# Performance work log

Hardware: AMD Instinct MI355X
Metric: run time of the kernel (lower is better)

Reference implementation:

```python
import jax, jax.numpy as jnp
import numpy as np

NUM_SINK = 8   # cfg.SINKHORN_ITERS
MASS = 0.9     # marginal value used for a and b


def _graph_conv(x, W_enc, b_enc, W1, b1, W2, b2, k):
    # Node encoder
    h = jax.nn.relu(x @ W_enc + b_enc)                       # [G,M,D]
    # kNN in embedding space (per graph)
    sq = jnp.sum(h * h, axis=-1)                             # [G,M]
    d2 = sq[:, :, None] + sq[:, None, :] - 2.0 * jnp.einsum('gmd,gnd->gmn', h, h)
    d2 = d2 + jnp.eye(h.shape[1], dtype=h.dtype) * 1e9       # exclude self-loop
    _, idx = jax.lax.top_k(-d2, k)                           # [G,M,k]
    neigh = jax.vmap(lambda hg, ig: hg[ig])(h, idx)          # [G,M,k,D]
    hc = jnp.broadcast_to(h[:, :, None, :], neigh.shape)
    e = jnp.concatenate([hc, neigh - hc], axis=-1)           # [G,M,k,2D]
    e = jax.nn.relu(e @ W1 + b1)                             # edge embed
    e = e @ W2 + b2                                          # back to D
    return jnp.max(e, axis=2)                                # max-aggregate over neighbors


def _sinkhorn(cost, lam):
    # log-domain unrolled Sinkhorn, batched over graphs; a=b=0.9 marginals
    log_p = -cost / lam                                      # [G,M,N]
    log_m = jnp.log(jnp.asarray(MASS, cost.dtype))
    for _ in range(NUM_SINK - 1):
        log_p = log_p - (jax.nn.logsumexp(log_p, axis=2, keepdims=True) - log_m)
        log_p = log_p - (jax.nn.logsumexp(log_p, axis=1, keepdims=True) - log_m)
    log_p = log_p - (jax.nn.logsumexp(log_p, axis=2, keepdims=True) - log_m)
    return jnp.exp(log_p)


def setup_inputs() -> dict:
    key = jax.random.key(0)
    ks = jax.random.split(key, 6)
    G, M, D = 64, 256, 256
    E = 256  # edge embed size
    inp = {
        'tra_x': jax.random.normal(ks[0], (G, M, D), jnp.float32),
        'det_x': jax.random.normal(ks[1], (G, M, D), jnp.float32),
        'W_enc': jax.random.normal(ks[2], (D, D), jnp.float32) / np.sqrt(D),
        'b_enc': jnp.zeros((D,), jnp.float32),
        'W1': jax.random.normal(ks[3], (2 * D, E), jnp.float32) / np.sqrt(2 * D),
        'b1': jnp.zeros((E,), jnp.float32),
        'W2': jax.random.normal(ks[4], (E, D), jnp.float32) / np.sqrt(E),
        'b2': jnp.zeros((D,), jnp.float32),
        'eplison': jnp.zeros((1,), jnp.float32),
        'k': 16,
    }
    return inp


def reference(tra_x, det_x, W_enc, b_enc, W1, b1, W2, b2, eplison, k):
    tra = _graph_conv(tra_x, W_enc, b_enc, W1, b1, W2, b2, k)  # [G,M,D]
    det = _graph_conv(det_x, W_enc, b_enc, W1, b1, W2, b2, k)  # [G,N,D]
    corr = jnp.einsum('gmd,gnd->gmn', tra, det)
    n1 = jnp.linalg.norm(tra, axis=-1)                         # [G,M]
    n2 = jnp.linalg.norm(det, axis=-1)                         # [G,N]
    cost = -corr / (n1[:, :, None] * n2[:, None, :])
    lam = jnp.exp(eplison[0]) + 0.03
    return _sinkhorn(cost, lam)                                # [G,M,N]
```

## Files before the change

### kernel.cpp

```cpp
#include <hip/hip_runtime.h>
#include <math.h>

#define NG 64
#define NM 256
#define ND 256
#define NK 16
#define NR (NG * NM)
#define NB 16

#define MASSF 0.9f

typedef __attribute__((ext_vector_type(8))) short bf16x8;
typedef __attribute__((ext_vector_type(4))) float f32x4;

static __device__ __forceinline__ short f2bf(float x) {
  union {
    float f;
    unsigned u;
  } v;
  v.f = x;
  unsigned r = v.u + 0x7FFFu + ((v.u >> 16) & 1u);
  return (short)(r >> 16);
}
static __device__ __forceinline__ float bf2f(short x) {
  union {
    unsigned u;
    float f;
  } v;
  v.u = ((unsigned)(unsigned short)x) << 16;
  return v.f;
}

__global__ __launch_bounds__(256) void prep_k(const float* __restrict__ W1,
                                              const float* __restrict__ b1,
                                              const float* __restrict__ W2,
                                              short* __restrict__ w2t, short* __restrict__ w1cat,
                                              float* __restrict__ biascat) {
  const int b = blockIdx.x, k = threadIdx.x;
  if (b < 256) {
    w2t[b * 256 + k] = f2bf(W2[(size_t)k * 256 + b]);
  } else {
    const int n = b - 256;
    float v;
    if (n < 256)
      v = W1[(size_t)k * 256 + n] - W1[(size_t)(k + 256) * 256 + n];
    else
      v = W1[(size_t)(k + 256) * 256 + (n - 256)];
    w1cat[(size_t)n * 256 + k] = f2bf(v);
    if (k == 0) biascat[n] = (n < 256) ? b1[n] : 0.f;
  }
}

__global__ __launch_bounds__(256) void gemm_nn2_k(const float* __restrict__ A,
                                                  const float* __restrict__ B,
                                                  const float* __restrict__ bias,
                                                  float* __restrict__ C,
                                                  short* __restrict__ Cbf) {
  __shared__ float As[2][16][68];
  __shared__ float Bs[2][16][128];
  const int tid = threadIdx.x;
  const int tx = tid & 15, ty = tid >> 4;
  const int m0 = blockIdx.y * 64, n0 = blockIdx.x * 128;
  const int arow = tid >> 2, akc = (tid & 3) * 4;
  const int bkr = tid >> 4, bcc = (tid & 15) * 4;
  float4 av, bv0, bv1;
  float acc[4][8] = {};
  auto gload = [&](int k0) {
    av = *(const float4*)&A[(size_t)(m0 + arow) * 256 + k0 + akc];
    bv0 = *(const float4*)&B[(size_t)(k0 + bkr) * 256 + n0 + bcc];
    bv1 = *(const float4*)&B[(size_t)(k0 + bkr) * 256 + n0 + 64 + bcc];
  };
  auto swrite = [&](int buf) {
    As[buf][akc + 0][arow] = av.x;
    As[buf][akc + 1][arow] = av.y;
    As[buf][akc + 2][arow] = av.z;
    As[buf][akc + 3][arow] = av.w;
    *(float4*)&Bs[buf][bkr][bcc] = bv0;
    *(float4*)&Bs[buf][bkr][64 + bcc] = bv1;
  };
  gload(0);
  swrite(0);
  __syncthreads();
  for (int s = 0; s < 16; ++s) {
    if (s < 15) gload((s + 1) * 16);
    const int buf = s & 1;
#pragma unroll
    for (int kk = 0; kk < 16; ++kk) {
      const float4 a0 = *(const float4*)&As[buf][kk][ty * 4];
      const float4 b0 = *(const float4*)&Bs[buf][kk][tx * 4];
      const float4 b1 = *(const float4*)&Bs[buf][kk][64 + tx * 4];
      const float aa[4] = {a0.x, a0.y, a0.z, a0.w};
      const float bb[8] = {b0.x, b0.y, b0.z, b0.w, b1.x, b1.y, b1.z, b1.w};
#pragma unroll
      for (int i = 0; i < 4; ++i)
#pragma unroll
        for (int j = 0; j < 8; ++j) acc[i][j] = fmaf(aa[i], bb[j], acc[i][j]);
    }
    if (s < 15) swrite((s + 1) & 1);
    __syncthreads();
  }
  const float4 bia0 = *(const float4*)&bias[n0 + tx * 4];
  const float4 bia1 = *(const float4*)&bias[n0 + 64 + tx * 4];
#pragma unroll
  for (int i = 0; i < 4; ++i) {
    const size_t row = (size_t)(m0 + ty * 4 + i);
    float4 o0 = {fmaxf(acc[i][0] + bia0.x, 0.f), fmaxf(acc[i][1] + bia0.y, 0.f),
                 fmaxf(acc[i][2] + bia0.z, 0.f), fmaxf(acc[i][3] + bia0.w, 0.f)};
    float4 o1 = {fmaxf(acc[i][4] + bia1.x, 0.f), fmaxf(acc[i][5] + bia1.y, 0.f),
                 fmaxf(acc[i][6] + bia1.z, 0.f), fmaxf(acc[i][7] + bia1.w, 0.f)};
    *(float4*)&C[row * 256 + n0 + tx * 4] = o0;
    *(float4*)&C[row * 256 + n0 + 64 + tx * 4] = o1;
    short4 h0 = {f2bf(o0.x), f2bf(o0.y), f2bf(o0.z), f2bf(o0.w)};
    short4 h1 = {f2bf(o1.x), f2bf(o1.y), f2bf(o1.z), f2bf(o1.w)};
    *(short4*)&Cbf[row * 256 + n0 + tx * 4] = h0;
    *(short4*)&Cbf[row * 256 + n0 + 64 + tx * 4] = h1;
  }
}

__global__ __launch_bounds__(256) void gemm_nt2_k(const float* __restrict__ h,
                                                  float* __restrict__ C) {
  const int flat0 = blockIdx.x + 2 * (blockIdx.y + 4 * blockIdx.z);
  const int flat = ((flat0 & 7) << 6) | (flat0 >> 3);
  const int bx = flat & 1, by = (flat >> 1) & 3, g = flat >> 3;
  if (bx == 0 && by >= 2) return;
  __shared__ float As[2][16][68];
  __shared__ float Bs[2][16][128];
  const float* Ag = h + (size_t)g * NM * ND;
  float* Cg = C + (size_t)g * NM * NM;
  const int tid = threadIdx.x;
  const int tx = tid & 15, ty = tid >> 4;
  const int m0 = by * 64, n0 = bx * 128;
  const int arow = tid >> 2, akc = (tid & 3) * 4;
  const int brow = tid >> 1, bkc = (tid & 1) * 8;
  float4 av, bva, bvb;
  float acc[4][8] = {};
  auto gload = [&](int k0) {
    av = *(const float4*)&Ag[(size_t)(m0 + arow) * 256 + k0 + akc];
    bva = *(const float4*)&Ag[(size_t)(n0 + brow) * 256 + k0 + bkc];
    bvb = *(const float4*)&Ag[(size_t)(n0 + brow) * 256 + k0 + bkc + 4];
  };
  auto swrite = [&](int buf) {
    As[buf][akc + 0][arow] = av.x;
    As[buf][akc + 1][arow] = av.y;
    As[buf][akc + 2][arow] = av.z;
    As[buf][akc + 3][arow] = av.w;
    Bs[buf][bkc + 0][brow] = bva.x;
    Bs[buf][bkc + 1][brow] = bva.y;
    Bs[buf][bkc + 2][brow] = bva.z;
    Bs[buf][bkc + 3][brow] = bva.w;
    Bs[buf][bkc + 4][brow] = bvb.x;
    Bs[buf][bkc + 5][brow] = bvb.y;
    Bs[buf][bkc + 6][brow] = bvb.z;
    Bs[buf][bkc + 7][brow] = bvb.w;
  };
  gload(0);
  swrite(0);
  __syncthreads();
  for (int s = 0; s < 16; ++s) {
    if (s < 15) gload((s + 1) * 16);
    const int buf = s & 1;
#pragma unroll
    for (int kk = 0; kk < 16; ++kk) {
      const float4 a0 = *(const float4*)&As[buf][kk][ty * 4];
      const float4 b0 = *(const float4*)&Bs[buf][kk][tx * 4];
      const float4 b1 = *(const float4*)&Bs[buf][kk][64 + tx * 4];
      const float aa[4] = {a0.x, a0.y, a0.z, a0.w};
      const float bb[8] = {b0.x, b0.y, b0.z, b0.w, b1.x, b1.y, b1.z, b1.w};
#pragma unroll
      for (int i = 0; i < 4; ++i)
#pragma unroll
        for (int j = 0; j < 8; ++j) acc[i][j] = fmaf(aa[i], bb[j], acc[i][j]);
    }
    if (s < 15) swrite((s + 1) & 1);
    __syncthreads();
  }
#pragma unroll
  for (int i = 0; i < 4; ++i) {
    const size_t row = (size_t)(m0 + ty * 4 + i);
    float4 o0 = {acc[i][0], acc[i][1], acc[i][2], acc[i][3]};
    float4 o1 = {acc[i][4], acc[i][5], acc[i][6], acc[i][7]};
    *(float4*)&Cg[row * 256 + n0 + tx * 4] = o0;
    *(float4*)&Cg[row * 256 + n0 + 64 + tx * 4] = o1;
  }
  if (bx == 1 && by < 2) {
#pragma unroll
    for (int j = 0; j < 4; ++j) {
      const size_t col0 = (size_t)(n0 + tx * 4 + j);
      const size_t col1 = (size_t)(n0 + 64 + tx * 4 + j);
      float4 t0 = {acc[0][j], acc[1][j], acc[2][j], acc[3][j]};
      float4 t1 = {acc[0][4 + j], acc[1][4 + j], acc[2][4 + j], acc[3][4 + j]};
      *(float4*)&Cg[col0 * 256 + m0 + ty * 4] = t0;
      *(float4*)&Cg[col1 * 256 + m0 + ty * 4] = t1;
    }
  }
}

__global__ __launch_bounds__(256) void diag_k(const float* __restrict__ S,
                                              float* __restrict__ sq) {
  const int g = blockIdx.x, m = threadIdx.x;
  sq[g * 256 + m] = S[(size_t)g * NM * NM + (size_t)m * 257];
}

__global__ __launch_bounds__(256, 2) void mlp1_mfma_k(const short* __restrict__ A,
                                                      const short* __restrict__ Bt,
                                                      const float* __restrict__ biascat,
                                                      short* __restrict__ baseb,
                                                      short* __restrict__ n1b) {
  __shared__ char As[64 * 512];
  const int tid = threadIdx.x;
  const int l = tid & 63, wv = tid >> 6;
  const int r = l & 15, gq = l >> 4;
  const int m0 = blockIdx.y * 64, n0 = blockIdx.x * 128;
  bf16x8 bfr[2][8];
  float bv[2];
#pragma unroll
  for (int nt = 0; nt < 2; ++nt) {
    const int col = n0 + wv * 32 + nt * 16 + r;
    const short* wb = Bt + (size_t)col * 256 + gq * 8;
#pragma unroll
    for (int ks = 0; ks < 8; ++ks) bfr[nt][ks] = *(const bf16x8*)(wb + ks * 32);
    bv[nt] = biascat[col];
  }
  const int row = tid >> 2, ch = tid & 3;
  const char* ag = (const char*)(A + (size_t)(m0 + row) * 256) + ch * 128;
  char* lb = As + row * 512;
#pragma unroll
  for (int j = 0; j < 8; ++j)
    *(bf16x8*)(lb + (((ch * 128 + j * 16)) ^ ((row & 7) << 4))) = *(const bf16x8*)(ag + j * 16);
  __syncthreads();
  f32x4 acc[4][2];
#pragma unroll
  for (int mt = 0; mt < 4; ++mt)
#pragma unroll
    for (int nt = 0; nt < 2; ++nt) acc[mt][nt] = (f32x4){0.f, 0.f, 0.f, 0.f};
#pragma unroll
  for (int ks = 0; ks < 8; ++ks) {
    bf16x8 a[4];
#pragma unroll
    for (int mt = 0; mt < 4; ++mt)
      a[mt] = *(const bf16x8*)(As + (mt * 16 + r) * 512 + ((gq * 16 + ks * 64) ^ ((r & 7) << 4)));
#pragma unroll
    for (int mt = 0; mt < 4; ++mt)
#pragma unroll
      for (int nt = 0; nt < 2; ++nt)
        acc[mt][nt] = __builtin_amdgcn_mfma_f32_16x16x32_bf16(a[mt], bfr[nt][ks], acc[mt][nt], 0, 0, 0);
  }
  short* dst = (n0 < 256) ? baseb : n1b;
  const int cb = (n0 < 256) ? n0 : n0 - 256;
#pragma unroll
  for (int mt = 0; mt < 4; ++mt)
#pragma unroll
    for (int nt = 0; nt < 2; ++nt) {
      const int col = cb + wv * 32 + nt * 16 + r;
#pragma unroll
      for (int reg = 0; reg < 4; ++reg) {
        const int rw = m0 + mt * 16 + gq * 4 + reg;
        dst[(size_t)rw * 256 + col] = f2bf(acc[mt][nt][reg] + bv[nt]);
      }
    }
}

__global__ __launch_bounds__(256, 2) void cost_mfma_k(const short* __restrict__ featT,
                                                      const short* __restrict__ featD,
                                                      const float* __restrict__ nA,
                                                      const float* __restrict__ nB,
                                                      const float* __restrict__ eps,
                                                      float* __restrict__ P) {
  __shared__ char As[64 * 512];
  const int g = blockIdx.z;
  const short* A = featT + (size_t)g * NM * ND;
  const short* Bt = featD + (size_t)g * NM * ND;
  const int tid = threadIdx.x;
  const int l = tid & 63, wv = tid >> 6;
  const int r = l & 15, gq = l >> 4;
  const int m0 = blockIdx.y * 64, n0 = blockIdx.x * 128;
  bf16x8 bfr[2][8];
  float rnb[2];
#pragma unroll
  for (int nt = 0; nt < 2; ++nt) {
    const int col = n0 + wv * 32 + nt * 16 + r;
    const short* wb = Bt + (size_t)col * 256 + gq * 8;
#pragma unroll
    for (int ks = 0; ks < 8; ++ks) bfr[nt][ks] = *(const bf16x8*)(wb + ks * 32);
    rnb[nt] = 1.0f / nB[g * NM + col];
  }
  const int row = tid >> 2, ch = tid & 3;
  const char* ag = (const char*)(A + (size_t)(m0 + row) * 256) + ch * 128;
  char* lb = As + row * 512;
#pragma unroll
  for (int j = 0; j < 8; ++j)
    *(bf16x8*)(lb + (((ch * 128 + j * 16)) ^ ((row & 7) << 4))) = *(const bf16x8*)(ag + j * 16);
  __syncthreads();
  f32x4 acc[4][2];
#pragma unroll
  for (int mt = 0; mt < 4; ++mt)
#pragma unroll
    for (int nt = 0; nt < 2; ++nt) acc[mt][nt] = (f32x4){0.f, 0.f, 0.f, 0.f};
#pragma unroll
  for (int ks = 0; ks < 8; ++ks) {
    bf16x8 a[4];
#pragma unroll
    for (int mt = 0; mt < 4; ++mt)
      a[mt] = *(const bf16x8*)(As + (mt * 16 + r) * 512 + ((gq * 16 + ks * 64) ^ ((r & 7) << 4)));
#pragma unroll
    for (int mt = 0; mt < 4; ++mt)
#pragma unroll
      for (int nt = 0; nt < 2; ++nt)
        acc[mt][nt] = __builtin_amdgcn_mfma_f32_16x16x32_bf16(a[mt], bfr[nt][ks], acc[mt][nt], 0, 0, 0);
  }
  const float inv_lam = 1.0f / (expf(eps[0]) + 0.03f);
#pragma unroll
  for (int mt = 0; mt < 4; ++mt) {
    float ria[4];
#pragma unroll
    for (int reg = 0; reg < 4; ++reg)
      ria[reg] = inv_lam / nA[g * NM + m0 + mt * 16 + gq * 4 + reg];
#pragma unroll
    for (int nt = 0; nt < 2; ++nt) {
      const int col = n0 + wv * 32 + nt * 16 + r;
#pragma unroll
      for (int reg = 0; reg < 4; ++reg) {
        const int rw = m0 + mt * 16 + gq * 4 + reg;
        P[(size_t)g * NM * NM + (size_t)rw * 256 + col] =
            expf(acc[mt][nt][reg] * ria[reg] * rnb[nt]);
      }
    }
  }
}

__global__ __launch_bounds__(256) void normrow_bf_k(const short* __restrict__ feat,
                                                    float* __restrict__ nrm) {
  const int w = threadIdx.x >> 6, lane = threadIdx.x & 63;
  const int row = blockIdx.x * 4 + w;
  const short4 v = *(const short4*)&feat[(size_t)row * ND + lane * 4];
  const float a = bf2f(v.x), b = bf2f(v.y), c = bf2f(v.z), d = bf2f(v.w);
  float s = a * a + b * b + c * c + d * d;
#pragma unroll
  for (int off = 32; off; off >>= 1) s += __shfl_xor(s, off);
  if (lane == 0) nrm[row] = sqrtf(s);
}

__global__ __launch_bounds__(256) void topk_k(const float* __restrict__ S,
                                              const float* __restrict__ sq,
                                              int* __restrict__ idx) {
  const int w = threadIdx.x >> 6, lane = threadIdx.x & 63;
  const int row = blockIdx.x * 4 + w;
  const int g = row >> 8, m = row & 255;
  const float* Srow = S + (size_t)row * NM;
  const float* sqg = sq + g * NM;
  const float sm = sqg[m];
  const float4 sv = *(const float4*)&Srow[lane * 4];
  const float4 qv = *(const float4*)&sqg[lane * 4];
  float cand[4] = {sm + qv.x - 2.f * sv.x, sm + qv.y - 2.f * sv.y, sm + qv.z - 2.f * sv.z,
                   sm + qv.w - 2.f * sv.w};
#pragma unroll
  for (int t = 0; t < 4; ++t)
    if (lane * 4 + t == m) cand[t] = 1e30f;
  for (int rnd = 0; rnd < NK; ++rnd) {
    float bvv = cand[0];
    int bi = lane * 4;
#pragma unroll
    for (int t = 1; t < 4; ++t)
      if (cand[t] < bvv) {
        bvv = cand[t];
        bi = lane * 4 + t;
      }
#pragma unroll
    for (int off = 1; off < 64; off <<= 1) {
      const float ov = __shfl_xor(bvv, off);
      const int oi = __shfl_xor(bi, off);
      if (ov < bvv || (ov == bvv && oi < bi)) {
        bvv = ov;
        bi = oi;
      }
    }
    if (lane == 0) idx[(size_t)row * NK + rnd] = bi;
    if ((bi >> 2) == lane) cand[bi & 3] = 1e30f;
  }
}

__global__ __launch_bounds__(512, 4) void edgemlp_mfma7_k(
    const short* __restrict__ baseb, const short* __restrict__ n1b, const int* __restrict__ idx,
    const short* __restrict__ w2t, const float* __restrict__ b2, short* __restrict__ featbf) {
  __shared__ short E[2][2][512 * 8];
  __shared__ int sidx[NB * NK];
  const int tid = threadIdx.x;
  const int l = tid & 63, wv = tid >> 6;
  const int blk = ((blockIdx.x & 7) << 7) | (blockIdx.x >> 3);
  const int node0 = blk * NB;
  const int g = node0 >> 8;
  const int r = l & 15, gq = l >> 4;
  if (tid < NB * NK) sidx[tid] = idx[(size_t)node0 * NK + tid];
  bf16x8 bfr[2][8];
  float b2v[2];
#pragma unroll
  for (int t = 0; t < 2; ++t) {
    const int nb = wv * 2 + t;
    const short* wb = w2t + (size_t)(nb * 16 + r) * 256 + gq * 8;
#pragma unroll
    for (int ks = 0; ks < 8; ++ks) bfr[t][ks] = *(const bf16x8*)(wb + ks * 32);
    b2v[t] = b2[nb * 16 + r];
  }
  __syncthreads();
  const int r_s = tid & 15;
  const int col_s = ((tid >> 6) * 32) + (((tid >> 4) & 3) * 8);
  bf16x8 bs0, ns0, bs1, ns1;
  auto sload = [&](int s) {
    const int na = s * 2;
    bs0 = *(const bf16x8*)(baseb + (((size_t)(node0 + na)) << 8) + col_s);
    ns0 = *(const bf16x8*)(n1b + ((((size_t)g << 8) + sidx[na * NK + r_s]) << 8) + col_s);
    bs1 = *(const bf16x8*)(baseb + (((size_t)(node0 + na + 1)) << 8) + col_s);
    ns1 = *(const bf16x8*)(n1b + ((((size_t)g << 8) + sidx[(na + 1) * NK + r_s]) << 8) + col_s);
  };
  auto swrite = [&](int s) {
    const int buf = s & 1;
    bf16x8 w0, w1;
#pragma unroll
    for (int q = 0; q < 8; ++q) {
      w0[q] = f2bf(fmaxf(bf2f(bs0[q]) + bf2f(ns0[q]), 0.f));
      w1[q] = f2bf(fmaxf(bf2f(bs1[q]) + bf2f(ns1[q]), 0.f));
    }
    *(bf16x8*)&E[buf][0][tid * 8] = w0;
    *(bf16x8*)&E[buf][1][tid * 8] = w1;
  };
  sload(0);
  swrite(0);
  __syncthreads();
  for (int s = 0; s < NB / 2; ++s) {
    if (s + 1 < NB / 2) sload(s + 1);
    const int buf = s & 1;
#pragma unroll
    for (int q = 0; q < 2; ++q) {
      const short* eb = &E[buf][q][0];
      f32x4 acc0 = (f32x4){0.f, 0.f, 0.f, 0.f};
      f32x4 acc1 = (f32x4){0.f, 0.f, 0.f, 0.f};
#pragma unroll
      for (int ks = 0; ks < 8; ++ks) {
        const bf16x8 a = *(const bf16x8*)(eb + ks * 512 + l * 8);
        acc0 = __builtin_amdgcn_mfma_f32_16x16x32_bf16(a, bfr[0][ks], acc0, 0, 0, 0);
        acc1 = __builtin_amdgcn_mfma_f32_16x16x32_bf16(a, bfr[1][ks], acc1, 0, 0, 0);
      }
      const int nd = node0 + s * 2 + q;
      float m0v = fmaxf(fmaxf(acc0[0], acc0[1]), fmaxf(acc0[2], acc0[3]));
      m0v = fmaxf(m0v, __shfl_xor(m0v, 16));
      m0v = fmaxf(m0v, __shfl_xor(m0v, 32));
      float m1v = fmaxf(fmaxf(acc1[0], acc1[1]), fmaxf(acc1[2], acc1[3]));
      m1v = fmaxf(m1v, __shfl_xor(m1v, 16));
      m1v = fmaxf(m1v, __shfl_xor(m1v, 32));
      if (gq == 0) {
        featbf[((size_t)nd << 8) + (wv * 2 + 0) * 16 + r] = f2bf(m0v + b2v[0]);
        featbf[((size_t)nd << 8) + (wv * 2 + 1) * 16 + r] = f2bf(m1v + b2v[1]);
      }
    }
    if (s + 1 < NB / 2) swrite(s + 1);
    __syncthreads();
  }
}

__global__ __launch_bounds__(1024) void sinkhorn_k(float* __restrict__ P) {
  __shared__ float red[16][256];
  __shared__ float scal[256];
  const int t = threadIdx.x;
  const int tc = t & 15;
  const int trw = t >> 4;
  const int wv = t >> 6, l = t & 63;
  float* Pg = P + (size_t)blockIdx.x * NM * NM;
  float p[4][16];
#pragma unroll
  for (int i = 0; i < 4; ++i)
#pragma unroll
    for (int q = 0; q < 4; ++q)
      *(f32x4*)&p[i][q * 4] = *(const f32x4*)&Pg[(size_t)(trw * 4 + i) * NM + tc * 16 + q * 4];

  auto rowpass = [&]() {
#pragma unroll
    for (int i = 0; i < 4; ++i) {
      float s = p[i][0];
#pragma unroll
      for (int j = 1; j < 16; ++j) s += p[i][j];
      s += __shfl_xor(s, 1);
      s += __shfl_xor(s, 2);
      s += __shfl_xor(s, 4);
      s += __shfl_xor(s, 8);
      const float sc = MASSF / s;
#pragma unroll
      for (int j = 0; j < 16; ++j) p[i][j] *= sc;
    }
  };
  auto colpass = [&]() {
    float tmp[16];
#pragma unroll
    for (int j = 0; j < 16; ++j) tmp[j] = ((p[0][j] + p[1][j]) + (p[2][j] + p[3][j]));
#pragma unroll
    for (int j = 0; j < 16; ++j) {
      tmp[j] += __shfl_xor(tmp[j], 16);
      tmp[j] += __shfl_xor(tmp[j], 32);
    }
    if (l < 16) {
#pragma unroll
      for (int q = 0; q < 4; ++q)
        *(f32x4*)&red[wv][l * 16 + q * 4] = *(const f32x4*)&tmp[q * 4];
    }
    __syncthreads();
    if (t < 256) {
      float s = red[0][t];
#pragma unroll
      for (int w = 1; w < 16; ++w) s += red[w][t];
      scal[t] = MASSF / s;
    }
    __syncthreads();
#pragma unroll
    for (int j = 0; j < 16; ++j) {
      const float sc = scal[tc * 16 + j];
#pragma unroll
      for (int i = 0; i < 4; ++i) p[i][j] *= sc;
    }
    __syncthreads();
  };
  for (int it = 0; it < 7; ++it) {
    rowpass();
    colpass();
  }
  rowpass();
#pragma unroll
  for (int i = 0; i < 4; ++i)
#pragma unroll
    for (int q = 0; q < 4; ++q)
      *(f32x4*)&Pg[(size_t)(trw * 4 + i) * NM + tc * 16 + q * 4] = *(const f32x4*)&p[i][q * 4];
}

extern "C" void kernel_launch(void* const* d_in, const int* in_sizes, int n_in, void* d_out,
                              int out_size, void* d_ws, size_t ws_size, hipStream_t stream) {
  const float* tra_x = (const float*)d_in[0];
  const float* det_x = (const float*)d_in[1];
  const float* W_enc = (const float*)d_in[2];
  const float* b_enc = (const float*)d_in[3];
  const float* W1 = (const float*)d_in[4];
  const float* b1 = (const float*)d_in[5];
  const float* W2 = (const float*)d_in[6];
  const float* b2 = (const float*)d_in[7];
  const float* eps = (const float*)d_in[8];
  float* out = (float*)d_out;

  const size_t SZ = (size_t)NR * ND;
  float* h = (float*)d_ws;
  short* hbf = (short*)(h + SZ);
  short* baseb = hbf + SZ;
  short* n1b = baseb + SZ;
  short* featT = n1b + SZ;
  short* featD = featT + SZ;
  float* sq = (float*)(featD + SZ);
  float* nT = sq + NR;
  float* nD = nT + NR;
  int* idx = (int*)(nD + NR);
  short* w2t = (short*)(idx + (size_t)NR * NK);
  short* w1cat = w2t + 256 * 256;
  float* biascat = (float*)(w1cat + 512 * 256);
  float* S = out;

  const float* xs[2] = {tra_x, det_x};
  short* feats[2] = {featT, featD};
  float* nrms[2] = {nT, nD};

  prep_k<<<768, 256, 0, stream>>>(W1, b1, W2, w2t, w1cat, biascat);
  for (int s2 = 0; s2 < 2; ++s2) {
    gemm_nn2_k<<<dim3(2, 256), 256, 0, stream>>>(xs[s2], W_enc, b_enc, h, hbf);
    mlp1_mfma_k<<<dim3(4, 256), 256, 0, stream>>>(hbf, w1cat, biascat, baseb, n1b);
    gemm_nt2_k<<<dim3(2, 4, NG), 256, 0, stream>>>(h, S);
    diag_k<<<NG, 256, 0, stream>>>(S, sq);
    topk_k<<<4096, 256, 0, stream>>>(S, sq, idx);
    edgemlp_mfma7_k<<<NR / NB, 512, 0, stream>>>(baseb, n1b, idx, w2t, b2, feats[s2]);
    normrow_bf_k<<<4096, 256, 0, stream>>>(feats[s2], nrms[s2]);
  }
  cost_mfma_k<<<dim3(2, 4, NG), 256, 0, stream>>>(featT, featD, nT, nD, eps, out);
  sinkhorn_k<<<NG, 1024, 0, stream>>>(out);
}
```

Baseline: 404.6 us.

## Switch MFMA path to fp16, fuse diag and row-norm kernels, widen edge blocks

Converts every bf16 intermediate and MFMA op to fp16. The edge ReLU now uses packed v_pk_add/v_pk_max f16 instructions instead of per-element bf16 unpack and repack. The diagonal extraction moves into the NT gemm epilogue, and the feature row norms are computed inside the edge-MLP kernel, removing the diag_k and normrow kernels (four launches and their memory passes). The edge-MLP block also processes 32 nodes instead of 16, which halves the grid and amortizes the per-block weight loads. fp16 has a narrower range than bf16, which could affect accuracy if intermediate values grow large.

```diff
diff --git a/kernel.cpp b/kernel.cpp
--- a/kernel.cpp
+++ b/kernel.cpp
@@ -6,39 +6,31 @@
 #define ND 256
 #define NK 16
 #define NR (NG * NM)
-#define NB 16
+#define NB 32
 
 #define MASSF 0.9f
 
-typedef __attribute__((ext_vector_type(8))) short bf16x8;
+typedef _Float16 f16;
+typedef __attribute__((ext_vector_type(8))) _Float16 f16x8;
+typedef __attribute__((ext_vector_type(4))) _Float16 f16x4;
 typedef __attribute__((ext_vector_type(4))) float f32x4;
-
-static __device__ __forceinline__ short f2bf(float x) {
-  union {
-    float f;
-    unsigned u;
-  } v;
-  v.f = x;
-  unsigned r = v.u + 0x7FFFu + ((v.u >> 16) & 1u);
-  return (short)(r >> 16);
-}
-static __device__ __forceinline__ float bf2f(short x) {
-  union {
-    unsigned u;
-    float f;
-  } v;
-  v.u = ((unsigned)(unsigned short)x) << 16;
-  return v.f;
+typedef __attribute__((ext_vector_type(4))) unsigned u32x4;
+
+static __device__ __forceinline__ unsigned pkrelu(unsigned a, unsigned b) {
+  unsigned r;
+  asm("v_pk_add_f16 %0, %1, %2" : "=v"(r) : "v"(a), "v"(b));
+  asm("v_pk_max_f16 %0, %1, %2" : "=v"(r) : "v"(r), "v"(0u));
+  return r;
 }
 
 __global__ __launch_bounds__(256) void prep_k(const float* __restrict__ W1,
                                               const float* __restrict__ b1,
                                               const float* __restrict__ W2,
-                                              short* __restrict__ w2t, short* __restrict__ w1cat,
+                                              f16* __restrict__ w2t, f16* __restrict__ w1cat,
                                               float* __restrict__ biascat) {
   const int b = blockIdx.x, k = threadIdx.x;
   if (b < 256) {
-    w2t[b * 256 + k] = f2bf(W2[(size_t)k * 256 + b]);
+    w2t[b * 256 + k] = (f16)W2[(size_t)k * 256 + b];
   } else {
     const int n = b - 256;
     float v;
@@ -46,7 +38,7 @@
       v = W1[(size_t)k * 256 + n] - W1[(size_t)(k + 256) * 256 + n];
     else
       v = W1[(size_t)(k + 256) * 256 + (n - 256)];
-    w1cat[(size_t)n * 256 + k] = f2bf(v);
+    w1cat[(size_t)n * 256 + k] = (f16)v;
     if (k == 0) biascat[n] = (n < 256) ? b1[n] : 0.f;
   }
 }
@@ -55,7 +47,7 @@
                                                   const float* __restrict__ B,
                                                   const float* __restrict__ bias,
                                                   float* __restrict__ C,
-                                                  short* __restrict__ Cbf) {
+                                                  f16* __restrict__ Cf) {
   __shared__ float As[2][16][68];
   __shared__ float Bs[2][16][128];
   const int tid = threadIdx.x;
@@ -110,15 +102,16 @@
                  fmaxf(acc[i][6] + bia1.z, 0.f), fmaxf(acc[i][7] + bia1.w, 0.f)};
     *(float4*)&C[row * 256 + n0 + tx * 4] = o0;
     *(float4*)&C[row * 256 + n0 + 64 + tx * 4] = o1;
-    short4 h0 = {f2bf(o0.x), f2bf(o0.y), f2bf(o0.z), f2bf(o0.w)};
-    short4 h1 = {f2bf(o1.x), f2bf(o1.y), f2bf(o1.z), f2bf(o1.w)};
-    *(short4*)&Cbf[row * 256 + n0 + tx * 4] = h0;
-    *(short4*)&Cbf[row * 256 + n0 + 64 + tx * 4] = h1;
+    f16x4 h0 = {(f16)o0.x, (f16)o0.y, (f16)o0.z, (f16)o0.w};
+    f16x4 h1 = {(f16)o1.x, (f16)o1.y, (f16)o1.z, (f16)o1.w};
+    *(f16x4*)&Cf[row * 256 + n0 + tx * 4] = h0;
+    *(f16x4*)&Cf[row * 256 + n0 + 64 + tx * 4] = h1;
   }
 }
 
 __global__ __launch_bounds__(256) void gemm_nt2_k(const float* __restrict__ h,
-                                                  float* __restrict__ C) {
+                                                  float* __restrict__ C,
+                                                  float* __restrict__ sq) {
   const int flat0 = blockIdx.x + 2 * (blockIdx.y + 4 * blockIdx.z);
   const int flat = ((flat0 & 7) << 6) | (flat0 >> 3);
   const int bx = flat & 1, by = (flat >> 1) & 3, g = flat >> 3;
@@ -174,13 +167,16 @@
     if (s < 15) swrite((s + 1) & 1);
     __syncthreads();
   }
+  const int c0 = n0 + tx * 4, c1 = n0 + 64 + tx * 4;
 #pragma unroll
   for (int i = 0; i < 4; ++i) {
-    const size_t row = (size_t)(m0 + ty * 4 + i);
+    const int row = m0 + ty * 4 + i;
     float4 o0 = {acc[i][0], acc[i][1], acc[i][2], acc[i][3]};
     float4 o1 = {acc[i][4], acc[i][5], acc[i][6], acc[i][7]};
-    *(float4*)&Cg[row * 256 + n0 + tx * 4] = o0;
-    *(float4*)&Cg[row * 256 + n0 + 64 + tx * 4] = o1;
+    *(float4*)&Cg[(size_t)row * 256 + c0] = o0;
+    *(float4*)&Cg[(size_t)row * 256 + c1] = o1;
+    if (row >= c0 && row < c0 + 4) sq[g * 256 + row] = acc[i][row - c0];
+    if (row >= c1 && row < c1 + 4) sq[g * 256 + row] = acc[i][4 + row - c1];
   }
   if (bx == 1 && by < 2) {
 #pragma unroll
@@ -195,30 +191,24 @@
   }
 }
 
-__global__ __launch_bounds__(256) void diag_k(const float* __restrict__ S,
-                                              float* __restrict__ sq) {
-  const int g = blockIdx.x, m = threadIdx.x;
-  sq[g * 256 + m] = S[(size_t)g * NM * NM + (size_t)m * 257];
-}
-
-__global__ __launch_bounds__(256, 2) void mlp1_mfma_k(const short* __restrict__ A,
-                                                      const short* __restrict__ Bt,
+__global__ __launch_bounds__(256, 2) void mlp1_mfma_k(const f16* __restrict__ A,
+                                                      const f16* __restrict__ Bt,
                                                       const float* __restrict__ biascat,
-                                                      short* __restrict__ baseb,
-                                                      short* __restrict__ n1b) {
+                                                      f16* __restrict__ baseb,
+                                                      f16* __restrict__ n1b) {
   __shared__ char As[64 * 512];
   const int tid = threadIdx.x;
   const int l = tid & 63, wv = tid >> 6;
   const int r = l & 15, gq = l >> 4;
   const int m0 = blockIdx.y * 64, n0 = blockIdx.x * 128;
-  bf16x8 bfr[2][8];
+  f16x8 bfr[2][8];
   float bv[2];
 #pragma unroll
   for (int nt = 0; nt < 2; ++nt) {
     const int col = n0 + wv * 32 + nt * 16 + r;
-    const short* wb = Bt + (size_t)col * 256 + gq * 8;
-#pragma unroll
-    for (int ks = 0; ks < 8; ++ks) bfr[nt][ks] = *(const bf16x8*)(wb + ks * 32);
+    const f16* wb = Bt + (size_t)col * 256 + gq * 8;
+#pragma unroll
+    for (int ks = 0; ks < 8; ++ks) bfr[nt][ks] = *(const f16x8*)(wb + ks * 32);
     bv[nt] = biascat[col];
   }
   const int row = tid >> 2, ch = tid & 3;
@@ -226,7 +216,7 @@
   char* lb = As + row * 512;
 #pragma unroll
   for (int j = 0; j < 8; ++j)
-    *(bf16x8*)(lb + (((ch * 128 + j * 16)) ^ ((row & 7) << 4))) = *(const bf16x8*)(ag + j * 16);
+    *(f16x8*)(lb + (((ch * 128 + j * 16)) ^ ((row & 7) << 4))) = *(const f16x8*)(ag + j * 16);
   __syncthreads();
   f32x4 acc[4][2];
 #pragma unroll
@@ -235,17 +225,17 @@
     for (int nt = 0; nt < 2; ++nt) acc[mt][nt] = (f32x4){0.f, 0.f, 0.f, 0.f};
 #pragma unroll
   for (int ks = 0; ks < 8; ++ks) {
-    bf16x8 a[4];
+    f16x8 a[4];
 #pragma unroll
     for (int mt = 0; mt < 4; ++mt)
-      a[mt] = *(const bf16x8*)(As + (mt * 16 + r) * 512 + ((gq * 16 + ks * 64) ^ ((r & 7) << 4)));
+      a[mt] = *(const f16x8*)(As + (mt * 16 + r) * 512 + ((gq * 16 + ks * 64) ^ ((r & 7) << 4)));
 #pragma unroll
     for (int mt = 0; mt < 4; ++mt)
 #pragma unroll
       for (int nt = 0; nt < 2; ++nt)
-        acc[mt][nt] = __builtin_amdgcn_mfma_f32_16x16x32_bf16(a[mt], bfr[nt][ks], acc[mt][nt], 0, 0, 0);
-  }
-  short* dst = (n0 < 256) ? baseb : n1b;
+        acc[mt][nt] = __builtin_amdgcn_mfma_f32_16x16x32_f16(a[mt], bfr[nt][ks], acc[mt][nt], 0, 0, 0);
+  }
+  f16* dst = (n0 < 256) ? baseb : n1b;
   const int cb = (n0 < 256) ? n0 : n0 - 256;
 #pragma unroll
   for (int mt = 0; mt < 4; ++mt)
@@ -255,33 +245,33 @@
 #pragma unroll
       for (int reg = 0; reg < 4; ++reg) {
         const int rw = m0 + mt * 16 + gq * 4 + reg;
-        dst[(size_t)rw * 256 + col] = f2bf(acc[mt][nt][reg] + bv[nt]);
+        dst[(size_t)rw * 256 + col] = (f16)(acc[mt][nt][reg] + bv[nt]);
       }
     }
 }
 
-__global__ __launch_bounds__(256, 2) void cost_mfma_k(const short* __restrict__ featT,
-                                                      const short* __restrict__ featD,
+__global__ __launch_bounds__(256, 2) void cost_mfma_k(const f16* __restrict__ featT,
+                                                      const f16* __restrict__ featD,
                                                       const float* __restrict__ nA,
                                                       const float* __restrict__ nB,
                                                       const float* __restrict__ eps,
                                                       float* __restrict__ P) {
   __shared__ char As[64 * 512];
   const int g = blockIdx.z;
-  const short* A = featT + (size_t)g * NM * ND;
-  const short* Bt = featD + (size_t)g * NM * ND;
+  const f16* A = featT + (size_t)g * NM * ND;
+  const f16* Bt = featD + (size_t)g * NM * ND;
   const int tid = threadIdx.x;
   const int l = tid & 63, wv = tid >> 6;
   const int r = l & 15, gq = l >> 4;
   const int m0 = blockIdx.y * 64, n0 = blockIdx.x * 128;
-  bf16x8 bfr[2][8];
+  f16x8 bfr[2][8];
   float rnb[2];
 #pragma unroll
   for (int nt = 0; nt < 2; ++nt) {
     const int col = n0 + wv * 32 + nt * 16 + r;
-    const short* wb = Bt + (size_t)col * 256 + gq * 8;
-#pragma unroll
-    for (int ks = 0; ks < 8; ++ks) bfr[nt][ks] = *(const bf16x8*)(wb + ks * 32);
+    const f16* wb = Bt + (size_t)col * 256 + gq * 8;
+#pragma unroll
+    for (int ks = 0; ks < 8; ++ks) bfr[nt][ks] = *(const f16x8*)(wb + ks * 32);
     rnb[nt] = 1.0f / nB[g * NM + col];
   }
   const int row = tid >> 2, ch = tid & 3;
@@ -289,7 +279,7 @@
   char* lb = As + row * 512;
 #pragma unroll
   for (int j = 0; j < 8; ++j)
-    *(bf16x8*)(lb + (((ch * 128 + j * 16)) ^ ((row & 7) << 4))) = *(const bf16x8*)(ag + j * 16);
+    *(f16x8*)(lb + (((ch * 128 + j * 16)) ^ ((row & 7) << 4))) = *(const f16x8*)(ag + j * 16);
   __syncthreads();
   f32x4 acc[4][2];
 #pragma unroll
@@ -298,15 +288,15 @@
     for (int nt = 0; nt < 2; ++nt) acc[mt][nt] = (f32x4){0.f, 0.f, 0.f, 0.f};
 #pragma unroll
   for (int ks = 0; ks < 8; ++ks) {
-    bf16x8 a[4];
+    f16x8 a[4];
 #pragma unroll
     for (int mt = 0; mt < 4; ++mt)
-      a[mt] = *(const bf16x8*)(As + (mt * 16 + r) * 512 + ((gq * 16 + ks * 64) ^ ((r & 7) << 4)));
+      a[mt] = *(const f16x8*)(As + (mt * 16 + r) * 512 + ((gq * 16 + ks * 64) ^ ((r & 7) << 4)));
 #pragma unroll
     for (int mt = 0; mt < 4; ++mt)
 #pragma unroll
       for (int nt = 0; nt < 2; ++nt)
-        acc[mt][nt] = __builtin_amdgcn_mfma_f32_16x16x32_bf16(a[mt], bfr[nt][ks], acc[mt][nt], 0, 0, 0);
+        acc[mt][nt] = __builtin_amdgcn_mfma_f32_16x16x32_f16(a[mt], bfr[nt][ks], acc[mt][nt], 0, 0, 0);
   }
   const float inv_lam = 1.0f / (expf(eps[0]) + 0.03f);
 #pragma unroll
@@ -326,18 +316,6 @@
       }
     }
   }
-}
-
-__global__ __launch_bounds__(256) void normrow_bf_k(const short* __restrict__ feat,
-                                                    float* __restrict__ nrm) {
-  const int w = threadIdx.x >> 6, lane = threadIdx.x & 63;
-  const int row = blockIdx.x * 4 + w;
-  const short4 v = *(const short4*)&feat[(size_t)row * ND + lane * 4];
-  const float a = bf2f(v.x), b = bf2f(v.y), c = bf2f(v.z), d = bf2f(v.w);
-  float s = a * a + b * b + c * c + d * d;
-#pragma unroll
-  for (int off = 32; off; off >>= 1) s += __shfl_xor(s, off);
-  if (lane == 0) nrm[row] = sqrtf(s);
 }
 
 __global__ __launch_bounds__(256) void topk_k(const float* __restrict__ S,
@@ -379,49 +357,51 @@
   }
 }
 
-__global__ __launch_bounds__(512, 4) void edgemlp_mfma7_k(
-    const short* __restrict__ baseb, const short* __restrict__ n1b, const int* __restrict__ idx,
-    const short* __restrict__ w2t, const float* __restrict__ b2, short* __restrict__ featbf) {
-  __shared__ short E[2][2][512 * 8];
+__global__ __launch_bounds__(512, 4) void edgemlp_mfma8_k(
+    const f16* __restrict__ baseb, const f16* __restrict__ n1b, const int* __restrict__ idx,
+    const f16* __restrict__ w2t, const float* __restrict__ b2, f16* __restrict__ featf,
+    float* __restrict__ nrm) {
+  __shared__ unsigned E[2][2][512 * 4];
   __shared__ int sidx[NB * NK];
+  __shared__ float normp[NB][8];
   const int tid = threadIdx.x;
   const int l = tid & 63, wv = tid >> 6;
-  const int blk = ((blockIdx.x & 7) << 7) | (blockIdx.x >> 3);
+  const int blk = ((blockIdx.x & 7) << 6) | (blockIdx.x >> 3);
   const int node0 = blk * NB;
   const int g = node0 >> 8;
   const int r = l & 15, gq = l >> 4;
-  if (tid < NB * NK) sidx[tid] = idx[(size_t)node0 * NK + tid];
-  bf16x8 bfr[2][8];
+  sidx[tid] = idx[(size_t)node0 * NK + tid];
+  f16x8 bfr[2][8];
   float b2v[2];
 #pragma unroll
   for (int t = 0; t < 2; ++t) {
     const int nb = wv * 2 + t;
-    const short* wb = w2t + (size_t)(nb * 16 + r) * 256 + gq * 8;
-#pragma unroll
-    for (int ks = 0; ks < 8; ++ks) bfr[t][ks] = *(const bf16x8*)(wb + ks * 32);
+    const f16* wb = w2t + (size_t)(nb * 16 + r) * 256 + gq * 8;
+#pragma unroll
+    for (int ks = 0; ks < 8; ++ks) bfr[t][ks] = *(const f16x8*)(wb + ks * 32);
     b2v[t] = b2[nb * 16 + r];
   }
   __syncthreads();
   const int r_s = tid & 15;
   const int col_s = ((tid >> 6) * 32) + (((tid >> 4) & 3) * 8);
-  bf16x8 bs0, ns0, bs1, ns1;
+  u32x4 bs0, ns0, bs1, ns1;
   auto sload = [&](int s) {
     const int na = s * 2;
-    bs0 = *(const bf16x8*)(baseb + (((size_t)(node0 + na)) << 8) + col_s);
-    ns0 = *(const bf16x8*)(n1b + ((((size_t)g << 8) + sidx[na * NK + r_s]) << 8) + col_s);
-    bs1 = *(const bf16x8*)(baseb + (((size_t)(node0 + na + 1)) << 8) + col_s);
-    ns1 = *(const bf16x8*)(n1b + ((((size_t)g << 8) + sidx[(na + 1) * NK + r_s]) << 8) + col_s);
+    bs0 = *(const u32x4*)(baseb + (((size_t)(node0 + na)) << 8) + col_s);
+    ns0 = *(const u32x4*)(n1b + ((((size_t)g << 8) + sidx[na * NK + r_s]) << 8) + col_s);
+    bs1 = *(const u32x4*)(baseb + (((size_t)(node0 + na + 1)) << 8) + col_s);
+    ns1 = *(const u32x4*)(n1b + ((((size_t)g << 8) + sidx[(na + 1) * NK + r_s]) << 8) + col_s);
   };
   auto swrite = [&](int s) {
     const int buf = s & 1;
-    bf16x8 w0, w1;
-#pragma unroll
-    for (int q = 0; q < 8; ++q) {
-      w0[q] = f2bf(fmaxf(bf2f(bs0[q]) + bf2f(ns0[q]), 0.f));
-      w1[q] = f2bf(fmaxf(bf2f(bs1[q]) + bf2f(ns1[q]), 0.f));
-    }
-    *(bf16x8*)&E[buf][0][tid * 8] = w0;
-    *(bf16x8*)&E[buf][1][tid * 8] = w1;
+    u32x4 w0, w1;
+#pragma unroll
+    for (int q = 0; q < 4; ++q) {
+      w0[q] = pkrelu(bs0[q], ns0[q]);
+      w1[q] = pkrelu(bs1[q], ns1[q]);
+    }
+    *(u32x4*)&E[buf][0][tid * 4] = w0;
+    *(u32x4*)&E[buf][1][tid * 4] = w1;
   };
   sload(0);
   swrite(0);
@@ -431,14 +411,14 @@
     const int buf = s & 1;
 #pragma unroll
     for (int q = 0; q < 2; ++q) {
-      const short* eb = &E[buf][q][0];
+      const char* eb = (const char*)&E[buf][q][0];
       f32x4 acc0 = (f32x4){0.f, 0.f, 0.f, 0.f};
       f32x4 acc1 = (f32x4){0.f, 0.f, 0.f, 0.f};
 #pragma unroll
       for (int ks = 0; ks < 8; ++ks) {
-        const bf16x8 a = *(const bf16x8*)(eb + ks * 512 + l * 8);
-        acc0 = __builtin_amdgcn_mfma_f32_16x16x32_bf16(a, bfr[0][ks], acc0, 0, 0, 0);
-        acc1 = __builtin_amdgcn_mfma_f32_16x16x32_bf16(a, bfr[1][ks], acc1, 0, 0, 0);
+        const f16x8 a = *(const f16x8*)(eb + ks * 1024 + l * 16);
+        acc0 = __builtin_amdgcn_mfma_f32_16x16x32_f16(a, bfr[0][ks], acc0, 0, 0, 0);
+        acc1 = __builtin_amdgcn_mfma_f32_16x16x32_f16(a, bfr[1][ks], acc1, 0, 0, 0);
       }
       const int nd = node0 + s * 2 + q;
       float m0v = fmaxf(fmaxf(acc0[0], acc0[1]), fmaxf(acc0[2], acc0[3]));
@@ -447,13 +427,28 @@
       float m1v = fmaxf(fmaxf(acc1[0], acc1[1]), fmaxf(acc1[2], acc1[3]));
       m1v = fmaxf(m1v, __shfl_xor(m1v, 16));
       m1v = fmaxf(m1v, __shfl_xor(m1v, 32));
+      const f16 h0 = (f16)(m0v + b2v[0]);
+      const f16 h1 = (f16)(m1v + b2v[1]);
       if (gq == 0) {
-        featbf[((size_t)nd << 8) + (wv * 2 + 0) * 16 + r] = f2bf(m0v + b2v[0]);
-        featbf[((size_t)nd << 8) + (wv * 2 + 1) * 16 + r] = f2bf(m1v + b2v[1]);
+        featf[((size_t)nd << 8) + (wv * 2 + 0) * 16 + r] = h0;
+        featf[((size_t)nd << 8) + (wv * 2 + 1) * 16 + r] = h1;
       }
+      const float o0 = (float)h0, o1 = (float)h1;
+      float ss = o0 * o0 + o1 * o1;
+      ss += __shfl_xor(ss, 1);
+      ss += __shfl_xor(ss, 2);
+      ss += __shfl_xor(ss, 4);
+      ss += __shfl_xor(ss, 8);
+      if (l == 0) normp[s * 2 + q][wv] = ss;
     }
     if (s + 1 < NB / 2) swrite(s + 1);
     __syncthreads();
+  }
+  if (tid < NB) {
+    float s = 0.f;
+#pragma unroll
+    for (int w = 0; w < 8; ++w) s += normp[tid][w];
+    nrm[node0 + tid] = sqrtf(s);
   }
 }
 
@@ -544,33 +539,31 @@
 
   const size_t SZ = (size_t)NR * ND;
   float* h = (float*)d_ws;
-  short* hbf = (short*)(h + SZ);
-  short* baseb = hbf + SZ;
-  short* n1b = baseb + SZ;
-  short* featT = n1b + SZ;
-  short* featD = featT + SZ;
+  f16* hf = (f16*)(h + SZ);
+  f16* baseb = hf + SZ;
+  f16* n1b = baseb + SZ;
+  f16* featT = n1b + SZ;
+  f16* featD = featT + SZ;
   float* sq = (float*)(featD + SZ);
   float* nT = sq + NR;
   float* nD = nT + NR;
   int* idx = (int*)(nD + NR);
-  short* w2t = (short*)(idx + (size_t)NR * NK);
-  short* w1cat = w2t + 256 * 256;
+  f16* w2t = (f16*)(idx + (size_t)NR * NK);
+  f16* w1cat = w2t + 256 * 256;
   float* biascat = (float*)(w1cat + 512 * 256);
   float* S = out;
 
   const float* xs[2] = {tra_x, det_x};
-  short* feats[2] = {featT, featD};
+  f16* feats[2] = {featT, featD};
   float* nrms[2] = {nT, nD};
 
   prep_k<<<768, 256, 0, stream>>>(W1, b1, W2, w2t, w1cat, biascat);
   for (int s2 = 0; s2 < 2; ++s2) {
-    gemm_nn2_k<<<dim3(2, 256), 256, 0, stream>>>(xs[s2], W_enc, b_enc, h, hbf);
-    mlp1_mfma_k<<<dim3(4, 256), 256, 0, stream>>>(hbf, w1cat, biascat, baseb, n1b);
-    gemm_nt2_k<<<dim3(2, 4, NG), 256, 0, stream>>>(h, S);
-    diag_k<<<NG, 256, 0, stream>>>(S, sq);
+    gemm_nn2_k<<<dim3(2, 256), 256, 0, stream>>>(xs[s2], W_enc, b_enc, h, hf);
+    mlp1_mfma_k<<<dim3(4, 256), 256, 0, stream>>>(hf, w1cat, biascat, baseb, n1b);
+    gemm_nt2_k<<<dim3(2, 4, NG), 256, 0, stream>>>(h, S, sq);
     topk_k<<<4096, 256, 0, stream>>>(S, sq, idx);
-    edgemlp_mfma7_k<<<NR / NB, 512, 0, stream>>>(baseb, n1b, idx, w2t, b2, feats[s2]);
-    normrow_bf_k<<<4096, 256, 0, stream>>>(feats[s2], nrms[s2]);
+    edgemlp_mfma8_k<<<NR / NB, 512, 0, stream>>>(baseb, n1b, idx, w2t, b2, feats[s2], nrms[s2]);
   }
   cost_mfma_k<<<dim3(2, 4, NG), 256, 0, stream>>>(featT, featD, nT, nD, eps, out);
   sinkhorn_k<<<NG, 1024, 0, stream>>>(out);
```

New measurement: 377.7 us. -6.7%, faster.
